# Kernel optimization log

Measured on AMD Instinct MI355X. Metric: run time of the kernel, lower is better.

## Reference

```python
import jax, jax.numpy as jnp
import numpy as np

EMBED_DIM = 512
SMOOTH = 4.0        # args.lambda_softmax
LAMBDA_LSE = 6.0    # args.lambda_lse
LEAKY_SLOPE = 0.1
EPS = 1e-8


def setup_inputs() -> dict:
    key = jax.random.key(0)
    k1, k2, k3 = jax.random.split(key, 3)
    n_contract, n_region = 32, 256
    n_law, max_len = 32, 256
    contracts = jax.random.normal(k1, (n_contract, n_region, EMBED_DIM), jnp.float32)
    laws = jax.random.normal(k2, (n_law, max_len, EMBED_DIM), jnp.float32)
    law_lens = jax.random.randint(k3, (n_law,), 128, max_len + 1, jnp.int32)
    return {"contracts": contracts, "laws": laws, "law_lens": law_lens}


def reference(contracts, laws, law_lens):
    # contracts: [C, R, D], laws: [N, L, D], law_lens: [N]
    n_law, max_len, d = laws.shape
    # mask[n, l] = 1 if word l is within law n's true length
    mask = (jnp.arange(max_len)[None, :] < law_lens[:, None]).astype(contracts.dtype)

    # attn = law @ contract^T / sqrt(D): [N, C, L, R]
    attn = jnp.einsum('nld,crd->nclr', laws, contracts) / jnp.sqrt(jnp.float32(d))
    attn = jax.nn.leaky_relu(attn, LEAKY_SLOPE)
    # l2norm over region dim (per law-word row)
    attn = attn / (jnp.linalg.norm(attn, axis=-1, keepdims=True) + EPS)
    attn = jax.nn.softmax(attn, axis=-1) * SMOOTH
    # zero out contributions from padded law words (ragged lengths)
    attn = attn * mask[:, None, :, None]

    # weighted_law: [N, C, R, D]
    wlaw = jnp.einsum('nld,nclr->ncrd', laws, attn)

    # cosine similarity along D: [N, C, R]
    w12 = jnp.sum(contracts[None] * wlaw, axis=-1)
    w1 = jnp.linalg.norm(contracts, axis=-1)[None]          # [1, C, R]
    w2 = jnp.linalg.norm(wlaw, axis=-1)                      # [N, C, R]
    sim = w12 / jnp.maximum(w1 * w2, EPS)

    # LogSumExp aggregation over regions -> [N, C]
    row_sim = jnp.log(jnp.sum(jnp.exp(sim * LAMBDA_LSE), axis=-1)) / LAMBDA_LSE
    # concatenate per-law columns -> [C, N]
    return row_sim.T
```

## Files before the change

kernel.cpp:

```cpp
#include <hip/hip_runtime.h>
#include <hip/hip_bf16.h>

#define CN 32
#define RN 256
#define DN 512
#define NN 32
#define LN 256

#define STAGE_OFF 131072
#define SMEM_TOTAL 163840

typedef short v8s __attribute__((ext_vector_type(8)));
typedef float v4f __attribute__((ext_vector_type(4)));
typedef const __attribute__((address_space(1))) void* gas1_t;
typedef __attribute__((address_space(3))) void* las3_t;

__device__ __forceinline__ void gl2lds16(const void* g, void* l) {
  __builtin_amdgcn_global_load_lds((gas1_t)g, (las3_t)l, 16, 0, 0);
}

__device__ __forceinline__ unsigned short f2bf(float x) {
  unsigned int u = __float_as_uint(x);
  u = (u + 0x7fffu + ((u >> 16) & 1u)) >> 16;
  return (unsigned short)u;
}
__device__ __forceinline__ float bf2f(unsigned short h) {
  return __uint_as_float(((unsigned int)h) << 16);
}

__device__ __forceinline__ unsigned int pkbf(float a, float b) {
  __hip_bfloat162 h = __float22bfloat162_rn(make_float2(a, b));
  unsigned int u;
  __builtin_memcpy(&u, &h, sizeof(u));
  return u;
}

__device__ __forceinline__ const v8s* stgFrag(const unsigned short* buf, int r,
                                              int quad) {
  return (const v8s*)(buf + r * 32 + ((quad ^ ((r >> 1) & 3)) << 3));
}

__device__ __forceinline__ int satIdx(int r, int col) {
  return (r << 8) | ((((col >> 3) ^ (r & 7)) << 3) | (col & 7));
}

__device__ __forceinline__ v8s ldFrag64(const float* buf, int r, int cp) {
  const float* p = buf + r * 64 + (((cp + r) & 7) << 3);
  const float4 x0 = ((const float4*)p)[0];
  const float4 x1 = ((const float4*)p)[1];
  unsigned short h[8];
  h[0] = f2bf(x0.x); h[1] = f2bf(x0.y); h[2] = f2bf(x0.z); h[3] = f2bf(x0.w);
  h[4] = f2bf(x1.x); h[5] = f2bf(x1.y); h[6] = f2bf(x1.z); h[7] = f2bf(x1.w);
  return *(v8s*)h;
}

__global__ __launch_bounds__(512) void setup_kernel(
    const float* __restrict__ con, const float* __restrict__ laws,
    unsigned short* __restrict__ lawsB, unsigned short* __restrict__ conB,
    float* __restrict__ cnorm, unsigned short* __restrict__ G) {
  extern __shared__ float slice[];
  const int bid = blockIdx.x;
  const int t = threadIdx.x;
  const int n = bid >> 3;
  const int m0 = (bid & 7) << 5;
  const int lane = t & 63;
  const int w = t >> 6;
  const int quad = lane >> 4;
  const int l16 = lane & 15;
  const int rg = w >> 2;
  const int cg = w & 3;
  const float* lawN = laws + n * (LN * DN);

#pragma unroll
  for (int i = 0; i < 8; ++i) {
    const int s = i * 512 + t;
    const int row = s >> 4;
    const int p = s & 15;
    const int srcCol = ((((p >> 1) - row) & 7) << 3) + ((p & 1) << 2);
    gl2lds16(lawN + row * DN + srcCol, (char*)slice + s * 16);
  }

#pragma unroll
  for (int p = 0; p < 4; ++p) {
    const int off = bid * 16384 + p * 4096 + t * 8;
    const float4* src = (const float4*)(laws + off);
    float4 x0 = src[0], x1 = src[1];
    unsigned short h[8];
    h[0] = f2bf(x0.x); h[1] = f2bf(x0.y); h[2] = f2bf(x0.z); h[3] = f2bf(x0.w);
    h[4] = f2bf(x1.x); h[5] = f2bf(x1.y); h[6] = f2bf(x1.z); h[7] = f2bf(x1.w);
    *(v8s*)(lawsB + off) = *(v8s*)h;
  }
#pragma unroll
  for (int p = 0; p < 4; ++p) {
    const int r = bid * 32 + p * 8 + w;
    const float4* src = (const float4*)(con + r * DN + lane * 8);
    float4 x0 = src[0], x1 = src[1];
    unsigned short h[8];
    h[0] = f2bf(x0.x); h[1] = f2bf(x0.y); h[2] = f2bf(x0.z); h[3] = f2bf(x0.w);
    h[4] = f2bf(x1.x); h[5] = f2bf(x1.y); h[6] = f2bf(x1.z); h[7] = f2bf(x1.w);
    *(v8s*)(conB + r * DN + lane * 8) = *(v8s*)h;
    float s = x0.x * x0.x + x0.y * x0.y + x0.z * x0.z + x0.w * x0.w +
              x1.x * x1.x + x1.y * x1.y + x1.z * x1.z + x1.w * x1.w;
#pragma unroll
    for (int m = 1; m < 64; m <<= 1) s += __shfl_xor(s, m, 64);
    if (lane == 0) cnorm[r] = sqrtf(s);
  }

  v4f acc[4];
#pragma unroll
  for (int b = 0; b < 4; ++b) acc[b] = (v4f){0.f, 0.f, 0.f, 0.f};

  for (int ch = 0; ch < 8; ++ch) {
    __syncthreads();
    if (ch < 7) {
      const int dk = (ch + 1) << 6;
      char* dst = (char*)slice + ((ch + 1) & 1) * 65536;
#pragma unroll
      for (int i = 0; i < 8; ++i) {
        const int s = i * 512 + t;
        const int row = s >> 4;
        const int p = s & 15;
        const int srcCol = ((((p >> 1) - row) & 7) << 3) + ((p & 1) << 2);
        gl2lds16(lawN + row * DN + dk + srcCol, dst + s * 16);
      }
    }
    const float* buf = slice + (ch & 1) * 16384;
#pragma unroll
    for (int step = 0; step < 2; ++step) {
      const int cp = quad + (step << 2);
      v8s af = ldFrag64(buf, m0 + rg * 16 + l16, cp);
#pragma unroll
      for (int ct = 0; ct < 4; ++ct) {
        v8s bf = ldFrag64(buf, cg * 64 + ct * 16 + l16, cp);
        acc[ct] = __builtin_amdgcn_mfma_f32_16x16x32_bf16(af, bf, acc[ct], 0, 0, 0);
      }
    }
  }
  unsigned short* g = G + n * (LN * LN);
#pragma unroll
  for (int ct = 0; ct < 4; ++ct)
#pragma unroll
    for (int reg = 0; reg < 4; ++reg) {
      const int l = m0 + rg * 16 + quad * 4 + reg;
      g[l * LN + cg * 64 + ct * 16 + l16] = f2bf(acc[ct][reg]);
    }
}

__global__ __launch_bounds__(512, 2) void main_kernel(
    const int* __restrict__ law_lens, const unsigned short* __restrict__ lawsB,
    const unsigned short* __restrict__ conB, const unsigned short* __restrict__ Gm,
    const float* __restrict__ cnorm, float* __restrict__ out) {
  extern __shared__ char smem[];
  unsigned short* sAt = (unsigned short*)smem;
  char* stage = smem + STAGE_OFF;

  const int bid = blockIdx.x;
  const int n = bid >> 5;
  const int c = bid & 31;
  const int t = threadIdx.x;
  const int lane = t & 63;
  const int w = t >> 6;
  const int quad = lane >> 4;
  const int l16 = lane & 15;
  const int sub = t & 3;
  const int rQ = t >> 2;
  const int subx = sub ^ ((rQ >> 1) & 3);
  const int len = law_lens[n];
  const int nCh = (len + 31) >> 5;
  const int nLt = (len + 15) >> 4;
  const bool active = (w * 32) < len;

  const unsigned short* lawN = lawsB + n * (LN * DN);
  const unsigned short* conC = conB + c * (RN * DN);
  const unsigned short* Gn = Gm + n * (LN * LN);

  float w12p[16];
#pragma unroll
  for (int i = 0; i < 16; ++i) w12p[i] = 0.f;

  {
    const unsigned short* a0p = lawN + (w * 32 + l16) * DN + quad * 8;
    const unsigned short* a1p = a0p + 16 * DN;

    v4f acc[2][16];
#pragma unroll
    for (int a = 0; a < 2; ++a)
#pragma unroll
      for (int b = 0; b < 16; ++b) acc[a][b] = (v4f){0.f, 0.f, 0.f, 0.f};

#pragma unroll
    for (int i = 0; i < 2; ++i)
      gl2lds16(conC + (i * 128 + rQ) * DN + subx * 8,
               stage + i * 8192 + t * 16);

    for (int ch = 0; ch < 16; ++ch) {
      const int dk = ch << 5;
      __syncthreads();
      v8s af0 = *(const v8s*)(a0p + dk);
      v8s af1 = *(const v8s*)(a1p + dk);
      __builtin_amdgcn_sched_barrier(0);
      if (ch < 15) {
        char* dst = stage + ((ch + 1) & 1) * 16384;
#pragma unroll
        for (int i = 0; i < 2; ++i)
          gl2lds16(conC + (i * 128 + rQ) * DN + (dk + 32) + subx * 8,
                   dst + i * 8192 + t * 16);
      }
      __builtin_amdgcn_sched_barrier(0);
      if (active) {
        const unsigned short* cs =
            (const unsigned short*)(stage + (ch & 1) * 16384);
#pragma unroll
        for (int rt = 0; rt < 16; ++rt) {
          v8s bf = *stgFrag(cs, rt * 16 + l16, quad);
          acc[0][rt] = __builtin_amdgcn_mfma_f32_16x16x32_bf16(af0, bf, acc[0][rt], 0, 0, 0);
          acc[1][rt] = __builtin_amdgcn_mfma_f32_16x16x32_bf16(af1, bf, acc[1][rt], 0, 0, 0);
        }
      }
    }

    __syncthreads();

#pragma unroll
    for (int i = 0; i < 2; ++i)
      gl2lds16(Gn + (i * 128 + rQ) * LN + subx * 8, stage + i * 8192 + t * 16);

    if (active) {
#pragma unroll
      for (int tl = 0; tl < 2; ++tl) {
        unsigned int pk[16][2];
        float a0s[16];
#pragma unroll
        for (int reg = 0; reg < 4; ++reg) {
          const int lg = w * 32 + tl * 16 + quad * 4 + reg;
          float ss = 0.f;
#pragma unroll
          for (int rt = 0; rt < 16; ++rt) {
            const float v = acc[tl][rt][reg] * 0.04419417382415922f;
            const float lv = v > 0.f ? v : 0.1f * v;
            ss += lv * lv;
          }
#pragma unroll
          for (int m = 1; m < 16; m <<= 1) ss += __shfl_xor(ss, m, 64);
          const float inv = 1.f / (sqrtf(ss) + 1e-8f);
          float e[16];
          float den = 0.f;
#pragma unroll
          for (int rt = 0; rt < 16; ++rt) {
            const float v = acc[tl][rt][reg] * 0.04419417382415922f;
            const float lv = v > 0.f ? v : 0.1f * v;
            e[rt] = __expf(lv * inv);
            den += e[rt];
          }
#pragma unroll
          for (int m = 1; m < 16; m <<= 1) den += __shfl_xor(den, m, 64);
          const float sc = (lg < len) ? 4.f / den : 0.f;
#pragma unroll
          for (int rt = 0; rt < 16; ++rt) {
            const float v = acc[tl][rt][reg] * 0.04419417382415922f;
            const float a = e[rt] * sc;
            w12p[rt] += a * v;
            if (reg & 1)
              pk[rt][reg >> 1] = pkbf(a0s[rt], a);
            else
              a0s[rt] = a;
          }
        }
        const int lg0 = w * 32 + tl * 16 + quad * 4;
#pragma unroll
        for (int rt = 0; rt < 16; ++rt)
          *(uint2*)(sAt + satIdx(rt * 16 + l16, lg0)) = *(uint2*)pk[rt];
      }
    } else {
      uint2 z;
      z.x = 0u;
      z.y = 0u;
#pragma unroll
      for (int tl = 0; tl < 2; ++tl) {
        const int lg0 = w * 32 + tl * 16 + quad * 4;
#pragma unroll
        for (int rt = 0; rt < 16; ++rt)
          *(uint2*)(sAt + satIdx(rt * 16 + l16, lg0)) = z;
      }
    }
  }

#pragma unroll
  for (int rt = 0; rt < 16; ++rt) {
    w12p[rt] += __shfl_xor(w12p[rt], 16, 64);
    w12p[rt] += __shfl_xor(w12p[rt], 32, 64);
  }

  float nsv[2][4];
  {
    v4f acc[2][16];
#pragma unroll
    for (int a = 0; a < 2; ++a)
#pragma unroll
      for (int b = 0; b < 16; ++b) acc[a][b] = (v4f){0.f, 0.f, 0.f, 0.f};

    for (int ch = 0; ch < nCh; ++ch) {
      const int lk = ch << 5;
      __syncthreads();
      v8s af0 = *(const v8s*)(sAt + satIdx(w * 32 + l16, lk + quad * 8));
      v8s af1 = *(const v8s*)(sAt + satIdx(w * 32 + 16 + l16, lk + quad * 8));
      __builtin_amdgcn_sched_barrier(0);
      if (ch < nCh - 1) {
        char* dst = stage + ((ch + 1) & 1) * 16384;
#pragma unroll
        for (int i = 0; i < 2; ++i)
          gl2lds16(Gn + (i * 128 + rQ) * LN + (lk + 32) + subx * 8,
                   dst + i * 8192 + t * 16);
      }
      __builtin_amdgcn_sched_barrier(0);
      const unsigned short* gs =
          (const unsigned short*)(stage + (ch & 1) * 16384);
#pragma unroll
      for (int lt = 0; lt < 16; ++lt) {
        if (lt < nLt) {
          v8s bf = *stgFrag(gs, lt * 16 + l16, quad);
          acc[0][lt] = __builtin_amdgcn_mfma_f32_16x16x32_bf16(af0, bf, acc[0][lt], 0, 0, 0);
          acc[1][lt] = __builtin_amdgcn_mfma_f32_16x16x32_bf16(af1, bf, acc[1][lt], 0, 0, 0);
        }
      }
    }
#pragma unroll
    for (int tl = 0; tl < 2; ++tl) {
#pragma unroll
      for (int reg = 0; reg < 4; ++reg) {
        const int r = w * 32 + tl * 16 + quad * 4 + reg;
        float s = 0.f;
#pragma unroll
        for (int lt = 0; lt < 16; ++lt) {
          if (lt < nLt)
            s += acc[tl][lt][reg] * bf2f(sAt[satIdx(r, lt * 16 + l16)]);
        }
#pragma unroll
        for (int m = 1; m < 16; m <<= 1) s += __shfl_xor(s, m, 64);
        nsv[tl][reg] = s;
      }
    }
  }

  float* w12s = (float*)stage;
  float* nsqS = (float*)(stage + 8192);
  float* red = (float*)(stage + 9216);
  __syncthreads();
  if (l16 == 0) {
#pragma unroll
    for (int tl = 0; tl < 2; ++tl)
#pragma unroll
      for (int reg = 0; reg < 4; ++reg)
        nsqS[w * 32 + tl * 16 + quad * 4 + reg] = nsv[tl][reg];
  }
  if (lane < 16) {
#pragma unroll
    for (int rt = 0; rt < 16; ++rt) w12s[w * 256 + rt * 16 + lane] = w12p[rt];
  }
  __syncthreads();
  float p = 0.f;
  if (t < 256) {
    float w12 = 0.f;
#pragma unroll
    for (int i = 0; i < 8; ++i) w12 += w12s[i * 256 + t];
    const float w1 = cnorm[c * RN + t];
    const float w2 = sqrtf(fmaxf(nsqS[t], 0.f));
    const float sim = (w12 * 22.627416997969522f) / fmaxf(w1 * w2, 1e-8f);
    p = __expf(6.f * sim);
  }
#pragma unroll
  for (int m = 1; m < 64; m <<= 1) p += __shfl_xor(p, m, 64);
  if (lane == 0) red[w] = p;
  __syncthreads();
  if (t == 0) {
    float s = 0.f;
#pragma unroll
    for (int i = 0; i < 8; ++i) s += red[i];
    out[c * NN + n] = logf(s) / 6.f;
  }
}

extern "C" void kernel_launch(void* const* d_in, const int* in_sizes, int n_in,
                              void* d_out, int out_size, void* d_ws, size_t ws_size,
                              hipStream_t stream) {
  (void)in_sizes; (void)n_in; (void)out_size;
  const float* contracts = (const float*)d_in[0];
  const float* laws = (const float*)d_in[1];
  const int* law_lens = (const int*)d_in[2];
  float* out = (float*)d_out;

  unsigned short* lawsB = (unsigned short*)d_ws;
  unsigned short* conB = lawsB + NN * LN * DN;
  unsigned short* G = conB + CN * RN * DN;
  float* cnorm = (float*)(G + NN * LN * LN);
  if (ws_size < (size_t)21004288) return;

  hipFuncSetAttribute((const void*)setup_kernel,
                      hipFuncAttributeMaxDynamicSharedMemorySize, 131072);
  hipFuncSetAttribute((const void*)main_kernel,
                      hipFuncAttributeMaxDynamicSharedMemorySize, SMEM_TOTAL);

  setup_kernel<<<256, 512, 131072, stream>>>(contracts, laws, lawsB, conB,
                                             cnorm, G);
  main_kernel<<<1024, 512, SMEM_TOTAL, stream>>>(law_lens, lawsB, conB, G,
                                                 cnorm, out);
}
```

Before: 264.9 us.

## Retile waves as 4x2 grid with 64-row A tiles and split-N cross-wave softmax

Each of the 8 waves now owns 64 law rows by 128 regions (and 64 regions by 128 L-cols in the second GEMM) instead of 32 rows by the full 256. Each B fragment read from LDS then feeds four MFMAs instead of two, roughly halving LDS fragment traffic. Because a row's softmax now spans two waves, row sums of squares and denominators are exchanged through shared memory with two extra barriers, and the exponentials are recomputed rather than kept in registers. The second GEMM also drops its ragged-length lt<nLt skip, so it always does the full work.

```diff
diff --git a/kernel.cpp b/kernel.cpp
--- a/kernel.cpp
+++ b/kernel.cpp
@@ -167,26 +167,31 @@
   const int subx = sub ^ ((rQ >> 1) & 3);
   const int len = law_lens[n];
   const int nCh = (len + 31) >> 5;
-  const int nLt = (len + 15) >> 4;
-  const bool active = (w * 32) < len;
+
+  const int wl = w & 3;
+  const int rh = w >> 2;
+  const bool active = (wl * 64) < len;
 
   const unsigned short* lawN = lawsB + n * (LN * DN);
   const unsigned short* conC = conB + c * (RN * DN);
   const unsigned short* Gn = Gm + n * (LN * LN);
 
-  float w12p[16];
-#pragma unroll
-  for (int i = 0; i < 16; ++i) w12p[i] = 0.f;
+  float* sSS = (float*)(stage + 16384);
+  float* sInv = (float*)(stage + 16384 + 2048);
+  float* sDen = (float*)(stage + 16384 + 3072);
+
+  float w12p[8];
+#pragma unroll
+  for (int i = 0; i < 8; ++i) w12p[i] = 0.f;
 
   {
-    const unsigned short* a0p = lawN + (w * 32 + l16) * DN + quad * 8;
-    const unsigned short* a1p = a0p + 16 * DN;
-
-    v4f acc[2][16];
-#pragma unroll
-    for (int a = 0; a < 2; ++a)
-#pragma unroll
-      for (int b = 0; b < 16; ++b) acc[a][b] = (v4f){0.f, 0.f, 0.f, 0.f};
+    const unsigned short* ap = lawN + (wl * 64 + l16) * DN + quad * 8;
+
+    v4f acc[4][8];
+#pragma unroll
+    for (int a = 0; a < 4; ++a)
+#pragma unroll
+      for (int b = 0; b < 8; ++b) acc[a][b] = (v4f){0.f, 0.f, 0.f, 0.f};
 
 #pragma unroll
     for (int i = 0; i < 2; ++i)
@@ -196,8 +201,10 @@
     for (int ch = 0; ch < 16; ++ch) {
       const int dk = ch << 5;
       __syncthreads();
-      v8s af0 = *(const v8s*)(a0p + dk);
-      v8s af1 = *(const v8s*)(a1p + dk);
+      v8s af0 = *(const v8s*)(ap + dk);
+      v8s af1 = *(const v8s*)(ap + 16 * DN + dk);
+      v8s af2 = *(const v8s*)(ap + 32 * DN + dk);
+      v8s af3 = *(const v8s*)(ap + 48 * DN + dk);
       __builtin_amdgcn_sched_barrier(0);
       if (ch < 15) {
         char* dst = stage + ((ch + 1) & 1) * 16384;
@@ -211,10 +218,12 @@
         const unsigned short* cs =
             (const unsigned short*)(stage + (ch & 1) * 16384);
 #pragma unroll
-        for (int rt = 0; rt < 16; ++rt) {
-          v8s bf = *stgFrag(cs, rt * 16 + l16, quad);
+        for (int rt = 0; rt < 8; ++rt) {
+          v8s bf = *stgFrag(cs, rh * 128 + rt * 16 + l16, quad);
           acc[0][rt] = __builtin_amdgcn_mfma_f32_16x16x32_bf16(af0, bf, acc[0][rt], 0, 0, 0);
           acc[1][rt] = __builtin_amdgcn_mfma_f32_16x16x32_bf16(af1, bf, acc[1][rt], 0, 0, 0);
+          acc[2][rt] = __builtin_amdgcn_mfma_f32_16x16x32_bf16(af2, bf, acc[2][rt], 0, 0, 0);
+          acc[3][rt] = __builtin_amdgcn_mfma_f32_16x16x32_bf16(af3, bf, acc[3][rt], 0, 0, 0);
         }
       }
     }
@@ -227,38 +236,64 @@
 
     if (active) {
 #pragma unroll
-      for (int tl = 0; tl < 2; ++tl) {
-        unsigned int pk[16][2];
-        float a0s[16];
+      for (int tl = 0; tl < 4; ++tl)
 #pragma unroll
         for (int reg = 0; reg < 4; ++reg) {
-          const int lg = w * 32 + tl * 16 + quad * 4 + reg;
+          const int lg = wl * 64 + tl * 16 + quad * 4 + reg;
           float ss = 0.f;
 #pragma unroll
-          for (int rt = 0; rt < 16; ++rt) {
+          for (int rt = 0; rt < 8; ++rt) {
             const float v = acc[tl][rt][reg] * 0.04419417382415922f;
             const float lv = v > 0.f ? v : 0.1f * v;
             ss += lv * lv;
           }
 #pragma unroll
           for (int m = 1; m < 16; m <<= 1) ss += __shfl_xor(ss, m, 64);
-          const float inv = 1.f / (sqrtf(ss) + 1e-8f);
-          float e[16];
+          if (l16 == 0) sSS[rh * 256 + lg] = ss;
+        }
+    }
+    __syncthreads();
+
+    if (active) {
+#pragma unroll
+      for (int tl = 0; tl < 4; ++tl)
+#pragma unroll
+        for (int reg = 0; reg < 4; ++reg) {
+          const int lg = wl * 64 + tl * 16 + quad * 4 + reg;
+          const float inv = 1.f / (sqrtf(sSS[lg] + sSS[256 + lg]) + 1e-8f);
           float den = 0.f;
 #pragma unroll
-          for (int rt = 0; rt < 16; ++rt) {
+          for (int rt = 0; rt < 8; ++rt) {
             const float v = acc[tl][rt][reg] * 0.04419417382415922f;
             const float lv = v > 0.f ? v : 0.1f * v;
-            e[rt] = __expf(lv * inv);
-            den += e[rt];
+            den += __expf(lv * inv);
           }
 #pragma unroll
           for (int m = 1; m < 16; m <<= 1) den += __shfl_xor(den, m, 64);
+          if (l16 == 0) {
+            sDen[rh * 256 + lg] = den;
+            if (rh == 0) sInv[lg] = inv;
+          }
+        }
+    }
+    __syncthreads();
+
+    if (active) {
+#pragma unroll
+      for (int tl = 0; tl < 4; ++tl) {
+        unsigned int pk[8][2];
+        float a0s[8];
+#pragma unroll
+        for (int reg = 0; reg < 4; ++reg) {
+          const int lg = wl * 64 + tl * 16 + quad * 4 + reg;
+          const float inv = sInv[lg];
+          const float den = sDen[lg] + sDen[256 + lg];
           const float sc = (lg < len) ? 4.f / den : 0.f;
 #pragma unroll
-          for (int rt = 0; rt < 16; ++rt) {
+          for (int rt = 0; rt < 8; ++rt) {
             const float v = acc[tl][rt][reg] * 0.04419417382415922f;
-            const float a = e[rt] * sc;
+            const float lv = v > 0.f ? v : 0.1f * v;
+            const float a = __expf(lv * inv) * sc;
             w12p[rt] += a * v;
             if (reg & 1)
               pk[rt][reg >> 1] = pkbf(a0s[rt], a);
@@ -266,44 +301,49 @@
               a0s[rt] = a;
           }
         }
-        const int lg0 = w * 32 + tl * 16 + quad * 4;
-#pragma unroll
-        for (int rt = 0; rt < 16; ++rt)
-          *(uint2*)(sAt + satIdx(rt * 16 + l16, lg0)) = *(uint2*)pk[rt];
+        const int lg0 = wl * 64 + tl * 16 + quad * 4;
+#pragma unroll
+        for (int rt = 0; rt < 8; ++rt)
+          *(uint2*)(sAt + satIdx(rh * 128 + rt * 16 + l16, lg0)) =
+              *(uint2*)pk[rt];
       }
     } else {
       uint2 z;
       z.x = 0u;
       z.y = 0u;
 #pragma unroll
-      for (int tl = 0; tl < 2; ++tl) {
-        const int lg0 = w * 32 + tl * 16 + quad * 4;
-#pragma unroll
-        for (int rt = 0; rt < 16; ++rt)
-          *(uint2*)(sAt + satIdx(rt * 16 + l16, lg0)) = z;
-      }
-    }
-  }
-
-#pragma unroll
-  for (int rt = 0; rt < 16; ++rt) {
+      for (int tl = 0; tl < 4; ++tl) {
+        const int lg0 = wl * 64 + tl * 16 + quad * 4;
+#pragma unroll
+        for (int rt = 0; rt < 8; ++rt)
+          *(uint2*)(sAt + satIdx(rh * 128 + rt * 16 + l16, lg0)) = z;
+      }
+    }
+  }
+
+#pragma unroll
+  for (int rt = 0; rt < 8; ++rt) {
     w12p[rt] += __shfl_xor(w12p[rt], 16, 64);
     w12p[rt] += __shfl_xor(w12p[rt], 32, 64);
   }
 
-  float nsv[2][4];
+  const int wr = w & 3;
+  const int lh = w >> 2;
+  float nsv[4][4];
   {
-    v4f acc[2][16];
-#pragma unroll
-    for (int a = 0; a < 2; ++a)
-#pragma unroll
-      for (int b = 0; b < 16; ++b) acc[a][b] = (v4f){0.f, 0.f, 0.f, 0.f};
+    v4f acc[4][8];
+#pragma unroll
+    for (int a = 0; a < 4; ++a)
+#pragma unroll
+      for (int b = 0; b < 8; ++b) acc[a][b] = (v4f){0.f, 0.f, 0.f, 0.f};
 
     for (int ch = 0; ch < nCh; ++ch) {
       const int lk = ch << 5;
       __syncthreads();
-      v8s af0 = *(const v8s*)(sAt + satIdx(w * 32 + l16, lk + quad * 8));
-      v8s af1 = *(const v8s*)(sAt + satIdx(w * 32 + 16 + l16, lk + quad * 8));
+      v8s af0 = *(const v8s*)(sAt + satIdx(wr * 64 + l16, lk + quad * 8));
+      v8s af1 = *(const v8s*)(sAt + satIdx(wr * 64 + 16 + l16, lk + quad * 8));
+      v8s af2 = *(const v8s*)(sAt + satIdx(wr * 64 + 32 + l16, lk + quad * 8));
+      v8s af3 = *(const v8s*)(sAt + satIdx(wr * 64 + 48 + l16, lk + quad * 8));
       __builtin_amdgcn_sched_barrier(0);
       if (ch < nCh - 1) {
         char* dst = stage + ((ch + 1) & 1) * 16384;
@@ -316,25 +356,24 @@
       const unsigned short* gs =
           (const unsigned short*)(stage + (ch & 1) * 16384);
 #pragma unroll
-      for (int lt = 0; lt < 16; ++lt) {
-        if (lt < nLt) {
-          v8s bf = *stgFrag(gs, lt * 16 + l16, quad);
-          acc[0][lt] = __builtin_amdgcn_mfma_f32_16x16x32_bf16(af0, bf, acc[0][lt], 0, 0, 0);
-          acc[1][lt] = __builtin_amdgcn_mfma_f32_16x16x32_bf16(af1, bf, acc[1][lt], 0, 0, 0);
-        }
-      }
-    }
-#pragma unroll
-    for (int tl = 0; tl < 2; ++tl) {
+      for (int lt = 0; lt < 8; ++lt) {
+        v8s bf = *stgFrag(gs, lh * 128 + lt * 16 + l16, quad);
+        acc[0][lt] = __builtin_amdgcn_mfma_f32_16x16x32_bf16(af0, bf, acc[0][lt], 0, 0, 0);
+        acc[1][lt] = __builtin_amdgcn_mfma_f32_16x16x32_bf16(af1, bf, acc[1][lt], 0, 0, 0);
+        acc[2][lt] = __builtin_amdgcn_mfma_f32_16x16x32_bf16(af2, bf, acc[2][lt], 0, 0, 0);
+        acc[3][lt] = __builtin_amdgcn_mfma_f32_16x16x32_bf16(af3, bf, acc[3][lt], 0, 0, 0);
+      }
+    }
+#pragma unroll
+    for (int tl = 0; tl < 4; ++tl) {
 #pragma unroll
       for (int reg = 0; reg < 4; ++reg) {
-        const int r = w * 32 + tl * 16 + quad * 4 + reg;
+        const int r = wr * 64 + tl * 16 + quad * 4 + reg;
         float s = 0.f;
 #pragma unroll
-        for (int lt = 0; lt < 16; ++lt) {
-          if (lt < nLt)
-            s += acc[tl][lt][reg] * bf2f(sAt[satIdx(r, lt * 16 + l16)]);
-        }
+        for (int lt = 0; lt < 8; ++lt)
+          s += acc[tl][lt][reg] *
+               bf2f(sAt[satIdx(r, lh * 128 + lt * 16 + l16)]);
 #pragma unroll
         for (int m = 1; m < 16; m <<= 1) s += __shfl_xor(s, m, 64);
         nsv[tl][reg] = s;
@@ -343,28 +382,28 @@
   }
 
   float* w12s = (float*)stage;
-  float* nsqS = (float*)(stage + 8192);
-  float* red = (float*)(stage + 9216);
+  float* nsqS2 = (float*)(stage + 4096);
+  float* red = (float*)(stage + 6144);
   __syncthreads();
   if (l16 == 0) {
 #pragma unroll
-    for (int tl = 0; tl < 2; ++tl)
+    for (int tl = 0; tl < 4; ++tl)
 #pragma unroll
       for (int reg = 0; reg < 4; ++reg)
-        nsqS[w * 32 + tl * 16 + quad * 4 + reg] = nsv[tl][reg];
+        nsqS2[lh * 256 + wr * 64 + tl * 16 + quad * 4 + reg] = nsv[tl][reg];
   }
   if (lane < 16) {
 #pragma unroll
-    for (int rt = 0; rt < 16; ++rt) w12s[w * 256 + rt * 16 + lane] = w12p[rt];
+    for (int rt = 0; rt < 8; ++rt)
+      w12s[wl * 256 + rh * 128 + rt * 16 + lane] = w12p[rt];
   }
   __syncthreads();
   float p = 0.f;
   if (t < 256) {
-    float w12 = 0.f;
-#pragma unroll
-    for (int i = 0; i < 8; ++i) w12 += w12s[i * 256 + t];
+    const float w12 =
+        w12s[t] + w12s[256 + t] + w12s[512 + t] + w12s[768 + t];
     const float w1 = cnorm[c * RN + t];
-    const float w2 = sqrtf(fmaxf(nsqS[t], 0.f));
+    const float w2 = sqrtf(fmaxf(nsqS2[t] + nsqS2[256 + t], 0.f));
     const float sim = (w12 * 22.627416997969522f) / fmaxf(w1 * w2, 1e-8f);
     p = __expf(6.f * sim);
   }
```

Result: slower. 309.0 us (+16.7%).

## Deepen first GEMM pipeline to a four-buffer ring with register-prefetched A fragments

Applied to the files above, without the earlier changes.

The law·contract GEMM stage now uses a four-slot LDS ring placed in the unused sAt region, issuing contract-tile loads three chunks ahead. Explicit vmcnt waits plus a raw s_barrier replace the per-chunk __syncthreads, and the law A fragments are double-buffered in registers. The MFMA loops are wrapped in s_setprio. In the second GEMM, the first two G chunks are prefetched before the loop and the per-tile nLt guard is dropped, so all 16 tiles are always computed and the padding is masked only in the reduction. This aims to hide global-load latency behind MFMA work, at the cost of fragile hand-counted vmcnt values and some wasted MFMAs on padded tiles.

```diff
diff --git a/kernel.cpp b/kernel.cpp
--- a/kernel.cpp
+++ b/kernel.cpp
@@ -152,6 +152,7 @@
     const float* __restrict__ cnorm, float* __restrict__ out) {
   extern __shared__ char smem[];
   unsigned short* sAt = (unsigned short*)smem;
+  char* abuf = smem;
   char* stage = smem + STAGE_OFF;
 
   const int bid = blockIdx.x;
@@ -167,7 +168,6 @@
   const int subx = sub ^ ((rQ >> 1) & 3);
   const int len = law_lens[n];
   const int nCh = (len + 31) >> 5;
-  const int nLt = (len + 15) >> 4;
   const bool active = (w * 32) < len;
 
   const unsigned short* lawN = lawsB + n * (LN * DN);
@@ -190,32 +190,65 @@
 
 #pragma unroll
     for (int i = 0; i < 2; ++i)
-      gl2lds16(conC + (i * 128 + rQ) * DN + subx * 8,
-               stage + i * 8192 + t * 16);
-
+      gl2lds16(conC + (i * 128 + rQ) * DN + 0 + subx * 8,
+               abuf + 0 * 16384 + i * 8192 + t * 16);
+    __builtin_amdgcn_sched_barrier(0);
+#pragma unroll
+    for (int i = 0; i < 2; ++i)
+      gl2lds16(conC + (i * 128 + rQ) * DN + 32 + subx * 8,
+               abuf + 1 * 16384 + i * 8192 + t * 16);
+    __builtin_amdgcn_sched_barrier(0);
+    v8s afC0 = *(const v8s*)(a0p);
+    v8s afC1 = *(const v8s*)(a1p);
+    __builtin_amdgcn_sched_barrier(0);
+#pragma unroll
+    for (int i = 0; i < 2; ++i)
+      gl2lds16(conC + (i * 128 + rQ) * DN + 64 + subx * 8,
+               abuf + 2 * 16384 + i * 8192 + t * 16);
+    __builtin_amdgcn_sched_barrier(0);
+
+#pragma unroll
     for (int ch = 0; ch < 16; ++ch) {
-      const int dk = ch << 5;
-      __syncthreads();
-      v8s af0 = *(const v8s*)(a0p + dk);
-      v8s af1 = *(const v8s*)(a1p + dk);
+      if (ch == 0)
+        asm volatile("s_waitcnt vmcnt(6)" ::: "memory");
+      else if (ch <= 13)
+        asm volatile("s_waitcnt vmcnt(8)" ::: "memory");
+      else if (ch == 14)
+        asm volatile("s_waitcnt vmcnt(6)" ::: "memory");
+      else
+        asm volatile("s_waitcnt vmcnt(4)" ::: "memory");
+      __builtin_amdgcn_s_barrier();
       __builtin_amdgcn_sched_barrier(0);
+      v8s afN0, afN1;
       if (ch < 15) {
-        char* dst = stage + ((ch + 1) & 1) * 16384;
+        const int dkn = (ch + 1) << 5;
+        afN0 = *(const v8s*)(a0p + dkn);
+        afN1 = *(const v8s*)(a1p + dkn);
+      }
+      if (ch + 3 < 16) {
+        const int dkn = (ch + 3) << 5;
+        char* dst = abuf + ((ch + 3) & 3) * 16384;
 #pragma unroll
         for (int i = 0; i < 2; ++i)
-          gl2lds16(conC + (i * 128 + rQ) * DN + (dk + 32) + subx * 8,
+          gl2lds16(conC + (i * 128 + rQ) * DN + dkn + subx * 8,
                    dst + i * 8192 + t * 16);
       }
       __builtin_amdgcn_sched_barrier(0);
       if (active) {
         const unsigned short* cs =
-            (const unsigned short*)(stage + (ch & 1) * 16384);
+            (const unsigned short*)(abuf + (ch & 3) * 16384);
+        __builtin_amdgcn_s_setprio(1);
 #pragma unroll
         for (int rt = 0; rt < 16; ++rt) {
           v8s bf = *stgFrag(cs, rt * 16 + l16, quad);
-          acc[0][rt] = __builtin_amdgcn_mfma_f32_16x16x32_bf16(af0, bf, acc[0][rt], 0, 0, 0);
-          acc[1][rt] = __builtin_amdgcn_mfma_f32_16x16x32_bf16(af1, bf, acc[1][rt], 0, 0, 0);
+          acc[0][rt] = __builtin_amdgcn_mfma_f32_16x16x32_bf16(afC0, bf, acc[0][rt], 0, 0, 0);
+          acc[1][rt] = __builtin_amdgcn_mfma_f32_16x16x32_bf16(afC1, bf, acc[1][rt], 0, 0, 0);
         }
+        __builtin_amdgcn_s_setprio(0);
+      }
+      if (ch < 15) {
+        afC0 = afN0;
+        afC1 = afN1;
       }
     }
 
@@ -224,6 +257,10 @@
 #pragma unroll
     for (int i = 0; i < 2; ++i)
       gl2lds16(Gn + (i * 128 + rQ) * LN + subx * 8, stage + i * 8192 + t * 16);
+#pragma unroll
+    for (int i = 0; i < 2; ++i)
+      gl2lds16(Gn + (i * 128 + rQ) * LN + 32 + subx * 8,
+               stage + 16384 + i * 8192 + t * 16);
 
     if (active) {
 #pragma unroll
@@ -299,13 +336,15 @@
 #pragma unroll
       for (int b = 0; b < 16; ++b) acc[a][b] = (v4f){0.f, 0.f, 0.f, 0.f};
 
+    __syncthreads();
+
     for (int ch = 0; ch < nCh; ++ch) {
       const int lk = ch << 5;
-      __syncthreads();
+      if (ch) __syncthreads();
       v8s af0 = *(const v8s*)(sAt + satIdx(w * 32 + l16, lk + quad * 8));
       v8s af1 = *(const v8s*)(sAt + satIdx(w * 32 + 16 + l16, lk + quad * 8));
       __builtin_amdgcn_sched_barrier(0);
-      if (ch < nCh - 1) {
+      if (ch > 0 && ch < nCh - 1) {
         char* dst = stage + ((ch + 1) & 1) * 16384;
 #pragma unroll
         for (int i = 0; i < 2; ++i)
@@ -315,14 +354,14 @@
       __builtin_amdgcn_sched_barrier(0);
       const unsigned short* gs =
           (const unsigned short*)(stage + (ch & 1) * 16384);
+      __builtin_amdgcn_s_setprio(1);
 #pragma unroll
       for (int lt = 0; lt < 16; ++lt) {
-        if (lt < nLt) {
-          v8s bf = *stgFrag(gs, lt * 16 + l16, quad);
-          acc[0][lt] = __builtin_amdgcn_mfma_f32_16x16x32_bf16(af0, bf, acc[0][lt], 0, 0, 0);
-          acc[1][lt] = __builtin_amdgcn_mfma_f32_16x16x32_bf16(af1, bf, acc[1][lt], 0, 0, 0);
-        }
-      }
+        v8s bf = *stgFrag(gs, lt * 16 + l16, quad);
+        acc[0][lt] = __builtin_amdgcn_mfma_f32_16x16x32_bf16(af0, bf, acc[0][lt], 0, 0, 0);
+        acc[1][lt] = __builtin_amdgcn_mfma_f32_16x16x32_bf16(af1, bf, acc[1][lt], 0, 0, 0);
+      }
+      __builtin_amdgcn_s_setprio(0);
     }
 #pragma unroll
     for (int tl = 0; tl < 2; ++tl) {
@@ -332,7 +371,7 @@
         float s = 0.f;
 #pragma unroll
         for (int lt = 0; lt < 16; ++lt) {
-          if (lt < nLt)
+          if ((lt << 4) < len)
             s += acc[tl][lt][reg] * bf2f(sAt[satIdx(r, lt * 16 + l16)]);
         }
 #pragma unroll
```

New measurement: 264.6 us. Within noise of the previous version (-0.1%).
